# Performance work log

Hardware: AMD Instinct MI355X
Metric: run time of the kernel (lower is better)

The kernel has to match this reference:

```python
import jax, jax.numpy as jnp
import numpy as np

BN_EPS = 1e-5

def setup_inputs() -> dict:
    key = jax.random.key(0)
    k1, k2 = jax.random.split(key)
    B, C, H, W, K = 256, 2048, 7, 7, 16
    featmap = jax.random.normal(k1, (B, C, H, W), dtype=jnp.float32)
    w16 = jax.random.normal(k2, (K, C), dtype=jnp.float32) * 0.02  # 1x1 conv weight
    bn_gamma = jnp.ones((K,), jnp.float32)
    bn_beta = jnp.zeros((K,), jnp.float32)
    bn_mean = jnp.zeros((K,), jnp.float32)
    bn_var = jnp.ones((K,), jnp.float32)
    return {"featmap": featmap, "w16": w16, "bn_gamma": bn_gamma,
            "bn_beta": bn_beta, "bn_mean": bn_mean, "bn_var": bn_var}

def reference(featmap, w16, bn_gamma, bn_beta, bn_mean, bn_var):
    # featmap: [B, 2048, 7, 7]; 1x1 conv -> featcov16: [B, 16, 7, 7]
    featcov16 = jnp.einsum('bchw,kc->bkhw', featmap, w16)
    # BatchNorm2d(16), inference-style with running stats
    inv = bn_gamma / jnp.sqrt(bn_var + BN_EPS)
    featcov16 = featcov16 * inv[None, :, None, None] + (bn_beta - bn_mean * inv)[None, :, None, None]
    # Loop-free bilinear pooling: original repeats featcov16[:,i] to 2048 ch,
    # multiplies with featmap, and AvgPool2d(7) -> mean over HxW.
    HW = featmap.shape[2] * featmap.shape[3]
    feat_matrix = jnp.einsum('bkhw,bchw->bkc', featcov16, featmap) / HW  # [B,16,2048]
    bp_out_feat = feat_matrix.reshape(feat_matrix.shape[0], -1)  # [B, 32768]
    return bp_out_feat
```

## Files before the change

### kernel.cpp

```cpp
#include <hip/hip_runtime.h>

#define BATCH 256
#define CDIM  2048
#define HW    49
#define KDIM  16


__global__ __launch_bounds__(256) void prep_kernel(
    const float* __restrict__ w16,
    const float* __restrict__ gamma, const float* __restrict__ beta,
    const float* __restrict__ mean,  const float* __restrict__ var,
    float* __restrict__ wT, float* __restrict__ pscr)
{
    const int idx = blockIdx.x * 256 + threadIdx.x;
    if (idx < CDIM * KDIM) {
        const int c = idx >> 4, k = idx & 15;
        const float inv = gamma[k] * rsqrtf(var[k] + 1e-5f) * (1.0f / 49.0f);
        wT[idx] = w16[k * CDIM + c] * inv;
    }
    for (int i = idx; i < BATCH * (HW * KDIM); i += 256 * 256) {
        const int k = i & 15;
        const float inv   = gamma[k] * rsqrtf(var[k] + 1e-5f);
        const float shift = (beta[k] - mean[k] * inv) * (1.0f / 49.0f);
        pscr[i] = shift;
    }
}

__global__ __launch_bounds__(512) void conv_kernel(
    const float* __restrict__ fm, const float* __restrict__ wT,
    float* __restrict__ pscr)
{
    __shared__ __align__(16) float wL[512 * KDIM];
    __shared__ float red[8 * KDIM * 52];

    const int tid  = threadIdx.x;
    const int b    = blockIdx.x >> 2;
    const int q    = blockIdx.x & 3;
    const int wav  = __builtin_amdgcn_readfirstlane(tid >> 6);
    const int lane = tid & 63;
    const int hwi  = lane < HW ? lane : HW - 1;

    {
        const float4* src = (const float4*)(wT + q * 512 * KDIM);
        float4* dst = (float4*)wL;
        #pragma unroll 4
        for (int i = tid; i < (512 * KDIM) / 4; i += 512) dst[i] = src[i];
    }
    __syncthreads();

    float acc[KDIM];
    #pragma unroll
    for (int k = 0; k < KDIM; ++k) acc[k] = 0.f;

    const float* fp = fm + (size_t)b * (CDIM * HW) + (size_t)(q * 512 + wav * 64) * HW + hwi;

    for (int g = 0; g < 64; g += 16) {
        float f[16];
        #pragma unroll
        for (int u = 0; u < 16; ++u)
            f[u] = fp[(g + u) * HW];
        #pragma unroll
        for (int u = 0; u < 16; ++u) {
            const float4* wrow = (const float4*)&wL[(wav * 64 + g + u) * KDIM];
            const float4 w0 = wrow[0];
            const float4 w1 = wrow[1];
            const float4 w2 = wrow[2];
            const float4 w3 = wrow[3];
            const float fv = f[u];
            acc[0]  += w0.x * fv; acc[1]  += w0.y * fv; acc[2]  += w0.z * fv; acc[3]  += w0.w * fv;
            acc[4]  += w1.x * fv; acc[5]  += w1.y * fv; acc[6]  += w1.z * fv; acc[7]  += w1.w * fv;
            acc[8]  += w2.x * fv; acc[9]  += w2.y * fv; acc[10] += w2.z * fv; acc[11] += w2.w * fv;
            acc[12] += w3.x * fv; acc[13] += w3.y * fv; acc[14] += w3.z * fv; acc[15] += w3.w * fv;
        }
    }

    if (lane < HW) {
        #pragma unroll
        for (int k = 0; k < KDIM; ++k)
            red[wav * (KDIM * 52) + k * 52 + lane] = acc[k];
    }
    __syncthreads();
    for (int j = tid; j < HW * KDIM; j += 512) {
        const int k = j / HW, hw = j - k * HW;
        float s = 0.f;
        #pragma unroll
        for (int w = 0; w < 8; ++w) s += red[w * (KDIM * 52) + k * 52 + hw];
        atomicAdd(&pscr[(size_t)b * (HW * KDIM) + hw * KDIM + k], s);
    }
}

__global__ __launch_bounds__(256) void bp_kernel(
    const float* __restrict__ fm, const float* __restrict__ pscr,
    float* __restrict__ out)
{
    __shared__ __align__(16) float fs[256 * HW];

    const int tid  = threadIdx.x;
    const int b    = blockIdx.x >> 1;
    const int half = blockIdx.x & 1;

    const float*  __restrict__ fmb = fm + (size_t)b * CDIM * HW;
    const float4* __restrict__ P4  = (const float4*)(pscr + (size_t)b * (HW * KDIM));

    for (int ch = 0; ch < 4; ++ch) {
        const int cb = half * 1024 + ch * 256;
        __syncthreads();
        {
            const float4* src = (const float4*)(fmb + (size_t)cb * HW);
            float4* dst = (float4*)fs;
            for (int i = tid; i < (256 * HW) / 4; i += 256) dst[i] = src[i];
        }
        __syncthreads();

        float acc[KDIM];
        #pragma unroll
        for (int k = 0; k < KDIM; ++k) acc[k] = 0.f;

        const float* row = fs + tid * HW;
        #pragma unroll 7
        for (int hw = 0; hw < HW; ++hw) {
            const float fv = row[hw];
            const float4 p0 = P4[hw * 4 + 0];
            const float4 p1 = P4[hw * 4 + 1];
            const float4 p2 = P4[hw * 4 + 2];
            const float4 p3 = P4[hw * 4 + 3];
            acc[0]  += p0.x * fv; acc[1]  += p0.y * fv; acc[2]  += p0.z * fv; acc[3]  += p0.w * fv;
            acc[4]  += p1.x * fv; acc[5]  += p1.y * fv; acc[6]  += p1.z * fv; acc[7]  += p1.w * fv;
            acc[8]  += p2.x * fv; acc[9]  += p2.y * fv; acc[10] += p2.z * fv; acc[11] += p2.w * fv;
            acc[12] += p3.x * fv; acc[13] += p3.y * fv; acc[14] += p3.z * fv; acc[15] += p3.w * fv;
        }

        float* ob = out + (size_t)b * (KDIM * CDIM) + cb + tid;
        #pragma unroll
        for (int kk = 0; kk < 16; ++kk) ob[kk * CDIM] = acc[kk];
    }
}

extern "C" void kernel_launch(void* const* d_in, const int* in_sizes, int n_in,
                              void* d_out, int out_size, void* d_ws, size_t ws_size,
                              hipStream_t stream) {
    const float* fm    = (const float*)d_in[0];
    const float* w16   = (const float*)d_in[1];
    const float* gamma = (const float*)d_in[2];
    const float* beta  = (const float*)d_in[3];
    const float* mean  = (const float*)d_in[4];
    const float* var   = (const float*)d_in[5];
    float* out  = (float*)d_out;
    float* wT   = (float*)d_ws;
    float* pscr = (float*)d_ws + CDIM * KDIM;

    prep_kernel<<<256, 256, 0, stream>>>(w16, gamma, beta, mean, var, wT, pscr);
    conv_kernel<<<BATCH * 4, 512, 0, stream>>>(fm, wT, pscr);
    bp_kernel<<<BATCH * 2, 256, 0, stream>>>(fm, pscr, out);
}
```

Before: 222.5 us.

## Restructure conv with vectorized HW tiling, drop atomics, add mid reduction kernel

The conv kernel now gives each lane four spatial positions as a vector, accumulates 16x4 outputs per lane, double-buffers the feature loads, and reduces across lanes with shuffles. Per-quarter partial sums go to scratch with plain stores instead of atomicAdd, and a new mid kernel sums them and applies the BN shift, which removes the scratch-initialisation pass from prep. The bp kernel is split into 8 blocks per batch, each handling one 256-channel chunk, to raise parallelism. The cost is an extra kernel launch, more scratch traffic, and higher register pressure in conv.

```diff
diff --git a/kernel.cpp b/kernel.cpp
--- a/kernel.cpp
+++ b/kernel.cpp
@@ -5,88 +5,136 @@
 #define HW    49
 #define KDIM  16
 
+typedef float f4u __attribute__((ext_vector_type(4), aligned(4)));
+
 
 __global__ __launch_bounds__(256) void prep_kernel(
     const float* __restrict__ w16,
-    const float* __restrict__ gamma, const float* __restrict__ beta,
-    const float* __restrict__ mean,  const float* __restrict__ var,
-    float* __restrict__ wT, float* __restrict__ pscr)
+    const float* __restrict__ gamma, const float* __restrict__ var,
+    float* __restrict__ wT)
 {
     const int idx = blockIdx.x * 256 + threadIdx.x;
-    if (idx < CDIM * KDIM) {
-        const int c = idx >> 4, k = idx & 15;
-        const float inv = gamma[k] * rsqrtf(var[k] + 1e-5f) * (1.0f / 49.0f);
-        wT[idx] = w16[k * CDIM + c] * inv;
-    }
-    for (int i = idx; i < BATCH * (HW * KDIM); i += 256 * 256) {
-        const int k = i & 15;
-        const float inv   = gamma[k] * rsqrtf(var[k] + 1e-5f);
-        const float shift = (beta[k] - mean[k] * inv) * (1.0f / 49.0f);
-        pscr[i] = shift;
-    }
+    const int c = idx >> 4, k = idx & 15;
+    const float inv = gamma[k] * rsqrtf(var[k] + 1e-5f) * (1.0f / 49.0f);
+    wT[idx] = w16[k * CDIM + c] * inv;
 }
 
-__global__ __launch_bounds__(512) void conv_kernel(
+__global__ __launch_bounds__(256, 3) void conv_kernel(
     const float* __restrict__ fm, const float* __restrict__ wT,
     float* __restrict__ pscr)
 {
     __shared__ __align__(16) float wL[512 * KDIM];
-    __shared__ float red[8 * KDIM * 52];
+    __shared__ __align__(16) float red[4 * 16 * 64];
 
     const int tid  = threadIdx.x;
     const int b    = blockIdx.x >> 2;
     const int q    = blockIdx.x & 3;
-    const int wav  = __builtin_amdgcn_readfirstlane(tid >> 6);
+    const int wav  = tid >> 6;
     const int lane = tid & 63;
-    const int hwi  = lane < HW ? lane : HW - 1;
+    const int cs   = lane >> 4;
+    const int h4   = lane & 15;
 
     {
         const float4* src = (const float4*)(wT + q * 512 * KDIM);
         float4* dst = (float4*)wL;
-        #pragma unroll 4
-        for (int i = tid; i < (512 * KDIM) / 4; i += 512) dst[i] = src[i];
+        for (int i = tid; i < (512 * KDIM) / 4; i += 256) dst[i] = src[i];
     }
     __syncthreads();
 
-    float acc[KDIM];
+    float4 acc[KDIM];
     #pragma unroll
-    for (int k = 0; k < KDIM; ++k) acc[k] = 0.f;
+    for (int k = 0; k < KDIM; ++k) acc[k] = make_float4(0.f, 0.f, 0.f, 0.f);
 
-    const float* fp = fm + (size_t)b * (CDIM * HW) + (size_t)(q * 512 + wav * 64) * HW + hwi;
+    const bool full = (h4 < 12);
+    const bool one  = (h4 == 12);
+    const float* fp0 = fm + (size_t)b * (CDIM * HW)
+                     + (size_t)(q * 512 + wav * 128 + cs) * HW + 4 * h4;
 
-    for (int g = 0; g < 64; g += 16) {
-        float f[16];
+#define LOADF(dst, ptr) do { f4u _v = {0.f, 0.f, 0.f, 0.f};                 \
+        if (full) _v = *(const f4u*)(ptr);                                   \
+        else if (one) _v.x = (ptr)[0];                                       \
+        (dst) = _v; } while (0)
+
+    f4u fbuf0, fbuf1, fbuf2, fbuf3, fnxt0, fnxt1, fnxt2, fnxt3;
+    LOADF(fbuf0, fp0 + 0 * (4 * HW));
+    LOADF(fbuf1, fp0 + 1 * (4 * HW));
+    LOADF(fbuf2, fp0 + 2 * (4 * HW));
+    LOADF(fbuf3, fp0 + 3 * (4 * HW));
+
+    for (int m = 0; m < 8; ++m) {
+        if (m < 7) {
+            const float* np = fp0 + (size_t)(m + 1) * 4 * (4 * HW);
+            LOADF(fnxt0, np + 0 * (4 * HW));
+            LOADF(fnxt1, np + 1 * (4 * HW));
+            LOADF(fnxt2, np + 2 * (4 * HW));
+            LOADF(fnxt3, np + 3 * (4 * HW));
+        }
+        const int lc0 = wav * 128 + m * 16 + cs;
         #pragma unroll
-        for (int u = 0; u < 16; ++u)
-            f[u] = fp[(g + u) * HW];
-        #pragma unroll
-        for (int u = 0; u < 16; ++u) {
-            const float4* wrow = (const float4*)&wL[(wav * 64 + g + u) * KDIM];
-            const float4 w0 = wrow[0];
-            const float4 w1 = wrow[1];
-            const float4 w2 = wrow[2];
-            const float4 w3 = wrow[3];
-            const float fv = f[u];
-            acc[0]  += w0.x * fv; acc[1]  += w0.y * fv; acc[2]  += w0.z * fv; acc[3]  += w0.w * fv;
-            acc[4]  += w1.x * fv; acc[5]  += w1.y * fv; acc[6]  += w1.z * fv; acc[7]  += w1.w * fv;
-            acc[8]  += w2.x * fv; acc[9]  += w2.y * fv; acc[10] += w2.z * fv; acc[11] += w2.w * fv;
-            acc[12] += w3.x * fv; acc[13] += w3.y * fv; acc[14] += w3.z * fv; acc[15] += w3.w * fv;
+        for (int u = 0; u < 4; ++u) {
+            const float4* wrow = (const float4*)&wL[(lc0 + u * 4) * KDIM];
+            float wv[16];
+            *(float4*)&wv[0]  = wrow[0];
+            *(float4*)&wv[4]  = wrow[1];
+            *(float4*)&wv[8]  = wrow[2];
+            *(float4*)&wv[12] = wrow[3];
+            const f4u f = (u == 0) ? fbuf0 : (u == 1) ? fbuf1 : (u == 2) ? fbuf2 : fbuf3;
+            #pragma unroll
+            for (int k = 0; k < KDIM; ++k) {
+                acc[k].x += wv[k] * f.x;
+                acc[k].y += wv[k] * f.y;
+                acc[k].z += wv[k] * f.z;
+                acc[k].w += wv[k] * f.w;
+            }
         }
+        fbuf0 = fnxt0; fbuf1 = fnxt1; fbuf2 = fnxt2; fbuf3 = fnxt3;
     }
+#undef LOADF
 
-    if (lane < HW) {
+#define RED1(V) { float v_ = (V); v_ += __shfl_xor(v_, 16); v_ += __shfl_xor(v_, 32); (V) = v_; }
+    #pragma unroll
+    for (int k = 0; k < KDIM; ++k) {
+        RED1(acc[k].x) RED1(acc[k].y) RED1(acc[k].z) RED1(acc[k].w)
+    }
+#undef RED1
+
+    if (lane < 16) {
         #pragma unroll
         for (int k = 0; k < KDIM; ++k)
-            red[wav * (KDIM * 52) + k * 52 + lane] = acc[k];
+            *(float4*)&red[(wav * 16 + k) * 64 + h4 * 4] = acc[k];
     }
     __syncthreads();
-    for (int j = tid; j < HW * KDIM; j += 512) {
-        const int k = j / HW, hw = j - k * HW;
-        float s = 0.f;
-        #pragma unroll
-        for (int w = 0; w < 8; ++w) s += red[w * (KDIM * 52) + k * 52 + hw];
-        atomicAdd(&pscr[(size_t)b * (HW * KDIM) + hw * KDIM + k], s);
+
+    for (int p = tid; p < HW * KDIM; p += 256) {
+        const int k = p / HW, hw = p - k * HW;
+        const int a = k * 64 + hw;
+        const float s = red[a] + red[a + 1024] + red[a + 2048] + red[a + 3072];
+        pscr[(size_t)(b * 4 + q) * 784 + p] = s;
     }
+}
+
+__global__ __launch_bounds__(256) void mid_kernel(
+    float* __restrict__ pscr,
+    const float* __restrict__ gamma, const float* __restrict__ beta,
+    const float* __restrict__ mean,  const float* __restrict__ var)
+{
+    const int tid  = threadIdx.x;
+    const size_t base = (size_t)blockIdx.x * (4 * 784);
+    float s0 = 0.f, s1 = 0.f, s2 = 0.f, s3 = 0.f;
+
+#define MIDR(SV, R) { const int j = tid + 256 * (R); if (j < 784) {          \
+        const int k = j & 15, hw = j >> 4;                                   \
+        const size_t src = base + k * HW + hw;                               \
+        const float t = pscr[src] + pscr[src + 784] + pscr[src + 1568] + pscr[src + 2352]; \
+        const float inv = gamma[k] * rsqrtf(var[k] + 1e-5f);                 \
+        SV = t + (beta[k] - mean[k] * inv) * (1.0f / 49.0f); } }
+    MIDR(s0, 0) MIDR(s1, 1) MIDR(s2, 2) MIDR(s3, 3)
+#undef MIDR
+    __syncthreads();
+    if (tid < 784)               pscr[base + tid]       = s0;
+    if (tid + 256 < 784)         pscr[base + tid + 256] = s1;
+    if (tid + 512 < 784)         pscr[base + tid + 512] = s2;
+    if (tid + 768 < 784)         pscr[base + tid + 768] = s3;
 }
 
 __global__ __launch_bounds__(256) void bp_kernel(
@@ -95,45 +143,40 @@
 {
     __shared__ __align__(16) float fs[256 * HW];
 
-    const int tid  = threadIdx.x;
-    const int b    = blockIdx.x >> 1;
-    const int half = blockIdx.x & 1;
+    const int tid = threadIdx.x;
+    const int b   = blockIdx.x >> 3;
+    const int oc  = (blockIdx.x & 7) * 256;
 
-    const float*  __restrict__ fmb = fm + (size_t)b * CDIM * HW;
-    const float4* __restrict__ P4  = (const float4*)(pscr + (size_t)b * (HW * KDIM));
+    {
+        const float4* src = (const float4*)(fm + ((size_t)b * CDIM + oc) * HW);
+        float4* dst = (float4*)fs;
+        for (int i = tid; i < (256 * HW) / 4; i += 256) dst[i] = src[i];
+    }
+    __syncthreads();
 
-    for (int ch = 0; ch < 4; ++ch) {
-        const int cb = half * 1024 + ch * 256;
-        __syncthreads();
-        {
-            const float4* src = (const float4*)(fmb + (size_t)cb * HW);
-            float4* dst = (float4*)fs;
-            for (int i = tid; i < (256 * HW) / 4; i += 256) dst[i] = src[i];
-        }
-        __syncthreads();
+    const float4* __restrict__ P4 = (const float4*)(pscr + (size_t)b * (4 * 784));
 
-        float acc[KDIM];
-        #pragma unroll
-        for (int k = 0; k < KDIM; ++k) acc[k] = 0.f;
+    float acc[KDIM];
+    #pragma unroll
+    for (int k = 0; k < KDIM; ++k) acc[k] = 0.f;
 
-        const float* row = fs + tid * HW;
-        #pragma unroll 7
-        for (int hw = 0; hw < HW; ++hw) {
-            const float fv = row[hw];
-            const float4 p0 = P4[hw * 4 + 0];
-            const float4 p1 = P4[hw * 4 + 1];
-            const float4 p2 = P4[hw * 4 + 2];
-            const float4 p3 = P4[hw * 4 + 3];
-            acc[0]  += p0.x * fv; acc[1]  += p0.y * fv; acc[2]  += p0.z * fv; acc[3]  += p0.w * fv;
-            acc[4]  += p1.x * fv; acc[5]  += p1.y * fv; acc[6]  += p1.z * fv; acc[7]  += p1.w * fv;
-            acc[8]  += p2.x * fv; acc[9]  += p2.y * fv; acc[10] += p2.z * fv; acc[11] += p2.w * fv;
-            acc[12] += p3.x * fv; acc[13] += p3.y * fv; acc[14] += p3.z * fv; acc[15] += p3.w * fv;
-        }
+    const float* row = fs + tid * HW;
+    #pragma unroll
+    for (int hw = 0; hw < HW; ++hw) {
+        const float fv = row[hw];
+        const float4 p0 = P4[hw * 4 + 0];
+        const float4 p1 = P4[hw * 4 + 1];
+        const float4 p2 = P4[hw * 4 + 2];
+        const float4 p3 = P4[hw * 4 + 3];
+        acc[0]  += p0.x * fv; acc[1]  += p0.y * fv; acc[2]  += p0.z * fv; acc[3]  += p0.w * fv;
+        acc[4]  += p1.x * fv; acc[5]  += p1.y * fv; acc[6]  += p1.z * fv; acc[7]  += p1.w * fv;
+        acc[8]  += p2.x * fv; acc[9]  += p2.y * fv; acc[10] += p2.z * fv; acc[11] += p2.w * fv;
+        acc[12] += p3.x * fv; acc[13] += p3.y * fv; acc[14] += p3.z * fv; acc[15] += p3.w * fv;
+    }
 
-        float* ob = out + (size_t)b * (KDIM * CDIM) + cb + tid;
-        #pragma unroll
-        for (int kk = 0; kk < 16; ++kk) ob[kk * CDIM] = acc[kk];
-    }
+    float* ob = out + (size_t)b * (KDIM * CDIM) + oc + tid;
+    #pragma unroll
+    for (int k = 0; k < KDIM; ++k) ob[k * CDIM] = acc[k];
 }
 
 extern "C" void kernel_launch(void* const* d_in, const int* in_sizes, int n_in,
@@ -149,7 +192,8 @@
     float* wT   = (float*)d_ws;
     float* pscr = (float*)d_ws + CDIM * KDIM;
 
-    prep_kernel<<<256, 256, 0, stream>>>(w16, gamma, beta, mean, var, wT, pscr);
-    conv_kernel<<<BATCH * 4, 512, 0, stream>>>(fm, wT, pscr);
-    bp_kernel<<<BATCH * 2, 256, 0, stream>>>(fm, pscr, out);
+    prep_kernel<<<128, 256, 0, stream>>>(w16, gamma, var, wT);
+    conv_kernel<<<BATCH * 4, 256, 0, stream>>>(fm, wT, pscr);
+    mid_kernel<<<BATCH, 256, 0, stream>>>(pscr, gamma, beta, mean, var);
+    bp_kernel<<<BATCH * 8, 256, 0, stream>>>(fm, pscr, out);
 }
```

New measurement: 234.0 us. 5.2% more time.
